# Kernel tuning notes

Hardware: AMD Instinct MI355X
Metric: run time of the kernel (lower is better)

The kernel has to match this reference:

```python
import jax, jax.numpy as jnp
import numpy as np

N = 100_000; E = 1_600_000; H = 64
TH = 0.7; ATT_TH = 0.2; EPS = 1e-5

# Heaviside spike with ATan surrogate gradient (spikingjelly default style).
@jax.custom_vjp
def spike_fn(v):
    return (v >= 0.0).astype(v.dtype)

def _spike_fwd(v):
    return spike_fn(v), v

def _spike_bwd(v, g):
    alpha = 2.0
    sg = (alpha / 2.0) / (1.0 + (jnp.pi / 2.0 * alpha * v) ** 2)
    return (g * sg,)

spike_fn.defvjp(_spike_fwd, _spike_bwd)

def lif_step(v, x, th):
    # integrate-and-fire step with hard reset-to-zero
    v = v + x
    s = spike_fn(v - th)
    return s, v * (1.0 - s)

def batchnorm(x, g, b):
    # training-mode BatchNorm1d over the node axis
    m = x.mean(axis=0)
    var = x.var(axis=0)
    return (x - m) * jax.lax.rsqrt(var + EPS) * g + b

def gcn(x, W, b, src, dst, w):
    # PyG GCNConv: xW, add self loops, symmetric deg^-1/2 normalization, scatter-add
    xw = x @ W                                   # [N,H]
    deg = jnp.ones((x.shape[0],), x.dtype).at[dst].add(w)   # self-loop weight 1
    dis = jax.lax.rsqrt(deg)
    norm = dis[src] * w * dis[dst]               # [E]
    agg = jnp.zeros_like(xw).at[dst].add(norm[:, None] * xw[src])
    return agg + (dis * dis)[:, None] * xw + b   # self-loop term + bias

def enc(x, src, dst, w, Wg, bg, bn_g, bn_b, v_conv):
    # Wg order: convs[0], conv, pos_conv, q_lins, k_lins, v_lins, att_conv
    # bn order:  bn_1, bn_2, pos_bn, pos_bn_2, q_bn, k_bn, v_bn, att_bn, att_bn_2
    x = batchnorm(gcn(x, Wg[0], bg[0], src, dst, w), bn_g[0], bn_b[0])
    x, v_conv = lif_step(v_conv, x, TH)          # conv_lif (stateful, never reset)
    x = batchnorm(gcn(x, Wg[1], bg[1], src, dst, w), bn_g[1], bn_b[1])
    z = jnp.zeros_like(x)
    # SGPE positional branch (pos_lif is reset after enc -> fresh state)
    x_pos_spike, _ = lif_step(z, x, TH)
    x_pos = batchnorm(gcn(x_pos_spike, Wg[2], bg[2], src, dst, w), bn_g[2], bn_b[2])
    x = batchnorm(x_pos + x, bn_g[3], bn_b[3])
    # attention branch: conv_lif second (stateful) call
    x_att, v_conv = lif_step(v_conv, x, TH)
    q, _ = lif_step(z, batchnorm(gcn(x_att, Wg[3], bg[3], src, dst, w), bn_g[4], bn_b[4]), TH)
    k, _ = lif_step(z, batchnorm(gcn(x_att, Wg[4], bg[4], src, dst, w), bn_g[5], bn_b[5]), TH)
    v, _ = lif_step(z, batchnorm(gcn(x_att, Wg[5], bg[5], src, dst, w), bn_g[6], bn_b[6]), TH)
    qk = (q * k).mean(axis=1)                    # [N]  (num_attention_heads == 1 path)
    qk, _ = lif_step(jnp.zeros_like(qk), qk, ATT_TH)
    att = qk[:, None] * v                        # repeat(H,1).T * v
    att = batchnorm(gcn(att, Wg[6], bg[6], src, dst, w), bn_g[7], bn_b[7])
    x = batchnorm(x + 0.125 * att, bn_g[8], bn_b[8])
    return x, v_conv

def setup_inputs():
    key = jax.random.key(0)
    ks = jax.random.split(key, 6)
    x = jax.random.normal(ks[0], (N, H), jnp.float32)
    edge_index = jax.random.randint(ks[1], (2, E), 0, N)
    edge_mask = jax.random.randint(ks[2], (E,), 0, 2, jnp.int32)
    Wg = jax.random.normal(ks[3], (7, H, H), jnp.float32) / jnp.sqrt(H)
    bg = jnp.zeros((7, H), jnp.float32)
    bn_g = jnp.ones((9, H), jnp.float32)
    bn_b = jnp.zeros((9, H), jnp.float32)
    W_lin = jax.random.normal(ks[4], (H, H), jnp.float32) / jnp.sqrt(H)
    return {"x": x, "edge_index": edge_index, "edge_mask": edge_mask,
            "Wg": Wg, "bg": bg, "bn_g": bn_g, "bn_b": bn_b, "W_lin": W_lin}

def reference(x, edge_index, edge_mask, Wg, bg, bn_g, bn_b, W_lin):
    src, dst = edge_index[0], edge_index[1]
    w1 = jnp.ones((E,), x.dtype)
    w2 = edge_mask.astype(x.dtype)   # dropout_edge(p=0.2) realized as fixed mask (weight 0 == removed edge)
    v0 = jnp.zeros((N, H), x.dtype)
    s1, v_conv = enc(x, src, dst, w1, Wg, bg, bn_g, bn_b, v0)
    s2, _ = enc(x, src, dst, w2, Wg, bg, bn_g, bn_b, v_conv)  # conv_lif state carries over
    z1 = (s1 @ W_lin).sum(axis=1)    # dec: lin(x).sum(1)
    z2 = (s2 @ W_lin).sum(axis=1)
    return (z1, z2)
```

## Files before the change

kernel.cpp:

```cpp
#include <hip/hip_runtime.h>
#include <math.h>
#include <stdint.h>
#include <limits.h>

#define NN 100000
#define NE 1600000
#define HH 64
#define THF 0.7f
#define ATTTH 0.2f
#define EPSF 1e-5f
#define SCAN_B ((NN + 255) / 256)
#define EM2CAP 1000000
#define NBE 2048
#define NHTOT ((size_t)NN * 64)
#define NB_ROW4C (NN / 4)
#define NTILE (NN / 32)

typedef unsigned long long u64;

__device__ inline int bcast_i(int v, int l) {
    return __builtin_amdgcn_readlane(v, l);
}
__device__ inline unsigned bcast_u(unsigned v, int l) {
    return (unsigned)__builtin_amdgcn_readlane((int)v, l);
}
__device__ inline float bcast_f(float v, int l) {
    return __int_as_float(__builtin_amdgcn_readlane(__float_as_int(v), l));
}


__global__ void hist_k(const int* __restrict__ dst, const int* __restrict__ mask,
                       int* __restrict__ cntp, int* __restrict__ rk) {
    int e = blockIdx.x * 256 + threadIdx.x;
    if (e >= NE) return;
    int d = dst[e];
    int inc = 1 | ((mask[e] & 1) << 16);
    rk[e] = atomicAdd(&cntp[d], inc);
}

__global__ void scan1d_k(const int* __restrict__ cntp,
                         int* __restrict__ rp1, int* __restrict__ rp2,
                         int* __restrict__ bsum,
                         float* __restrict__ dis1, float* __restrict__ d21,
                         float* __restrict__ dis2m, float* __restrict__ d22) {
    __shared__ int ls[256];
    int half = (blockIdx.x >= SCAN_B) ? 1 : 0;
    int blk = blockIdx.x - half * SCAN_B;
    int* rp = half ? rp2 : rp1;
    int i = blk * 256 + threadIdx.x;
    int p = (i < NN) ? cntp[i] : 0;
    int v = half ? (p >> 16) : (p & 0xFFFF);
    if (i < NN) {
        float dg = (float)(v + 1);
        float is = 1.0f / sqrtf(dg);
        float iv = 1.0f / dg;
        if (half) { dis2m[i] = is; d22[i] = iv; }
        else      { dis1[i] = is;  d21[i] = iv; }
    }
    ls[threadIdx.x] = v;
    __syncthreads();
    for (int off = 1; off < 256; off <<= 1) {
        int t = (threadIdx.x >= off) ? ls[threadIdx.x - off] : 0;
        __syncthreads();
        ls[threadIdx.x] += t;
        __syncthreads();
    }
    if (i < NN) rp[i] = ls[threadIdx.x] - v;
    if (threadIdx.x == 255) bsum[blockIdx.x] = ls[255];
}

__global__ __launch_bounds__(512) void scan2d_k(int* __restrict__ bsum,
                                                int* __restrict__ rp1,
                                                int* __restrict__ rp2) {
    __shared__ int ls[512];
    int i = threadIdx.x;
    for (int s = 0; s < 2; s++) {
        int v = (i < SCAN_B) ? bsum[s * SCAN_B + i] : 0;
        ls[i] = v;
        __syncthreads();
        for (int off = 1; off < 512; off <<= 1) {
            int t = (i >= off) ? ls[i - off] : 0;
            __syncthreads();
            ls[i] += t;
            __syncthreads();
        }
        if (i < SCAN_B) bsum[s * SCAN_B + i] = ls[i] - v;
        if (i == SCAN_B - 1) { if (s == 0) rp1[NN] = ls[i]; else rp2[NN] = ls[i]; }
        __syncthreads();
    }
}

__global__ void scan3d_k(int* __restrict__ rp1, int* __restrict__ rp2,
                         const int* __restrict__ bsum) {
    int half = (blockIdx.x >= SCAN_B) ? 1 : 0;
    int blk = blockIdx.x - half * SCAN_B;
    int* rp = half ? rp2 : rp1;
    int i = blk * 256 + threadIdx.x;
    if (i < NN) rp[i] += bsum[blockIdx.x];
}

__global__ void csr_fill_k(const int* __restrict__ src, const int* __restrict__ dst,
                           const int* __restrict__ mask, const int* __restrict__ rk,
                           const int* __restrict__ rp1, const int* __restrict__ rp2,
                           int* __restrict__ emA, int* __restrict__ emB) {
    int e = blockIdx.x * 256 + threadIdx.x;
    if (e >= NE) return;
    int s = src[e], d = dst[e];
    int mk = mask[e] & 1;
    int r = rk[e];
    emA[rp1[d] + (r & 0xFFFF)] = (s << 1) | mk;
    if (mk) emB[rp2[d] + (r >> 16)] = s;
}

__device__ void seg_sort_node(int* __restrict__ em, int beg, int end,
                              int* skey, int lane) {
    int L = end - beg;
    if (L <= 1) return;
    if (L <= 64) {
        int k = (lane < L) ? em[beg + lane] : INT_MAX;
        int rank = 0;
#pragma unroll 8
        for (int r = 0; r < L; r++) {
            int kr = bcast_i(k, r);
            rank += (kr < k || (kr == k && r < lane)) ? 1 : 0;
        }
        if (lane < L) em[beg + rank] = k;
    } else if (L <= 512) {
        for (int i = lane; i < L; i += 64) skey[i] = em[beg + i];
        for (int it = 0; it < L; it++) {
            int par = it & 1;
            for (int p = par + 2 * lane; p + 1 < L; p += 128) {
                int ka = skey[p], kb = skey[p + 1];
                if (kb < ka) { skey[p] = kb; skey[p + 1] = ka; }
            }
        }
        for (int i = lane; i < L; i += 64) em[beg + i] = skey[i];
    }
}

__global__ __launch_bounds__(256) void seg_sort2_k(int* __restrict__ emA,
                                                   const int* __restrict__ rp1,
                                                   int* __restrict__ emB,
                                                   const int* __restrict__ rp2) {
    __shared__ int skey[4][512];
    int tid = threadIdx.x, lane = tid & 63, w = tid >> 6;
    int bid = blockIdx.x;
    if (bid < NB_ROW4C) {
        int n = bid * 4 + w;
        seg_sort_node(emA, rp1[n], rp1[n + 1], skey[w], lane);
    } else {
        int n = (bid - NB_ROW4C) * 4 + w;
        seg_sort_node(emB, rp2[n], rp2[n + 1], skey[w], lane);
    }
}


__global__ __launch_bounds__(256) void gemm_k(const float* __restrict__ in,
                                              const float* __restrict__ W,
                                              float* __restrict__ xw) {
    __shared__ float sW[64 * 64];
    __shared__ float sx[32 * 65];
    int tid = threadIdx.x;
    const float4* W4 = (const float4*)W;
    float4* sW4 = (float4*)sW;
    for (int i = tid; i < 1024; i += 256) sW4[i] = W4[i];
    const float* inb = in + (size_t)blockIdx.x * 2048;
    for (int i = tid; i < 2048; i += 256) sx[(i >> 6) * 65 + (i & 63)] = inb[i];
    __syncthreads();
    int cg = tid & 15, rr = tid >> 4;
    float a0 = 0, a1 = 0, a2 = 0, a3 = 0, c0 = 0, c1 = 0, c2 = 0, c3 = 0;
#pragma unroll
    for (int k = 0; k < 64; k++) {
        float4 wv = *(const float4*)&sW[k * 64 + cg * 4];
        float xa = sx[rr * 65 + k];
        float xb = sx[(rr + 16) * 65 + k];
        a0 += xa * wv.x; a1 += xa * wv.y; a2 += xa * wv.z; a3 += xa * wv.w;
        c0 += xb * wv.x; c1 += xb * wv.y; c2 += xb * wv.z; c3 += xb * wv.w;
    }
    size_t r0 = (size_t)(blockIdx.x * 32 + rr) * 64 + cg * 4;
    size_t r1 = (size_t)(blockIdx.x * 32 + rr + 16) * 64 + cg * 4;
    *(float4*)&xw[r0] = make_float4(a0, a1, a2, a3);
    *(float4*)&xw[r1] = make_float4(c0, c1, c2, c3);
}


__global__ __launch_bounds__(256) void gather_stats_k(const float* __restrict__ xw,
                                                      const int* __restrict__ em,
                                                      int shift,
                                                      const float* __restrict__ dis,
                                                      const int* __restrict__ rp,
                                                      const float* __restrict__ d2i,
                                                      const float* __restrict__ bias,
                                                      float* __restrict__ out,
                                                      double* __restrict__ part) {
    int tid = threadIdx.x, lane = tid & 63, w = tid >> 6;
    double ps = 0.0, pq = 0.0;
    for (int n = blockIdx.x * 4 + w; n < NN; n += NBE * 4) {
        int beg = rp[n], end = rp[n + 1];
        float disn = dis[n];
        float self = d2i[n] * xw[(size_t)n * 64 + lane] + bias[lane];
        float acc = 0.0f;
        for (int base = beg; base < end; base += 64) {
            int cnt = min(64, end - base);
            int m = 0; float nl = 0.0f;
            if (base + lane < end) {
                m = em[base + lane];
                nl = dis[m >> shift] * disn;
            }
            int j = 0;
            for (; j + 8 <= cnt; j += 8) {
#pragma unroll
                for (int u = 0; u < 8; u++) {
                    int s = bcast_i(m, j + u) >> shift;
                    float nv = bcast_f(nl, j + u);
                    acc += nv * xw[(size_t)s * 64 + lane];
                }
            }
            for (; j < cnt; j++) {
                int s = bcast_i(m, j) >> shift;
                float nv = bcast_f(nl, j);
                acc += nv * xw[(size_t)s * 64 + lane];
            }
        }
        float o = acc + self;
        out[(size_t)n * 64 + lane] = o;
        ps += (double)o;
        pq += (double)o * (double)o;
    }
    __shared__ double ls[4][64], lq[4][64];
    ls[w][lane] = ps; lq[w][lane] = pq;
    __syncthreads();
    if (tid < 64) {
        double a = ls[0][tid] + ls[1][tid] + ls[2][tid] + ls[3][tid];
        double b = lq[0][tid] + lq[1][tid] + lq[2][tid] + lq[3][tid];
        part[(size_t)blockIdx.x * 128 + tid] = a;
        part[(size_t)blockIdx.x * 128 + 64 + tid] = b;
    }
}

__global__ __launch_bounds__(256) void sharedL0_k(const float* __restrict__ xw,
                                                  const int* __restrict__ em,
                                                  const int* __restrict__ rp,
                                                  const float* __restrict__ dis1,
                                                  const float* __restrict__ dis2m,
                                                  const float* __restrict__ d21,
                                                  const float* __restrict__ d22,
                                                  const float* __restrict__ bias,
                                                  float* __restrict__ o1,
                                                  float* __restrict__ o2,
                                                  double* __restrict__ part) {
    int tid = threadIdx.x, lane = tid & 63, w = tid >> 6;
    double sA = 0.0, qA = 0.0, sB = 0.0, qB = 0.0;
    for (int n = blockIdx.x * 4 + w; n < NN; n += NBE * 4) {
        int beg = rp[n], end = rp[n + 1];
        float disn1 = dis1[n], disn2 = dis2m[n];
        float xv = xw[(size_t)n * 64 + lane];
        float self1 = d21[n] * xv + bias[lane];
        float self2 = d22[n] * xv + bias[lane];
        float acc1 = 0.0f, acc2 = 0.0f;
        for (int base = beg; base < end; base += 64) {
            int cnt = min(64, end - base);
            int m = 0; float nl1 = 0.0f, nl2 = 0.0f;
            if (base + lane < end) {
                m = em[base + lane];
                int s = m >> 1;
                nl1 = dis1[s] * disn1;
                nl2 = dis2m[s] * disn2;
            }
            int j = 0;
            for (; j + 8 <= cnt; j += 8) {
#pragma unroll
                for (int u = 0; u < 8; u++) {
                    int key = bcast_i(m, j + u);
                    int s = key >> 1;
                    float n1 = bcast_f(nl1, j + u);
                    float n2 = bcast_f(nl2, j + u);
                    float v = xw[(size_t)s * 64 + lane];
                    acc1 += n1 * v;
                    acc2 += (key & 1) ? n2 * v : 0.0f;
                }
            }
            for (; j < cnt; j++) {
                int key = bcast_i(m, j);
                int s = key >> 1;
                float n1 = bcast_f(nl1, j);
                float n2 = bcast_f(nl2, j);
                float v = xw[(size_t)s * 64 + lane];
                acc1 += n1 * v;
                acc2 += (key & 1) ? n2 * v : 0.0f;
            }
        }
        size_t o = (size_t)n * 64 + lane;
        float v1 = acc1 + self1;
        float v2 = acc2 + self2;
        o1[o] = v1;
        o2[o] = v2;
        sA += (double)v1; qA += (double)v1 * (double)v1;
        sB += (double)v2; qB += (double)v2 * (double)v2;
    }
    __shared__ double l1[4][64], l2[4][64], l3[4][64], l4[4][64];
    l1[w][lane] = sA; l2[w][lane] = qA; l3[w][lane] = sB; l4[w][lane] = qB;
    __syncthreads();
    if (tid < 64) {
        size_t o = (size_t)blockIdx.x * 256;
        part[o + tid]       = l1[0][tid] + l1[1][tid] + l1[2][tid] + l1[3][tid];
        part[o + 64 + tid]  = l2[0][tid] + l2[1][tid] + l2[2][tid] + l2[3][tid];
        part[o + 128 + tid] = l3[0][tid] + l3[1][tid] + l3[2][tid] + l3[3][tid];
        part[o + 192 + tid] = l4[0][tid] + l4[1][tid] + l4[2][tid] + l4[3][tid];
    }
}


__global__ __launch_bounds__(256) void bitagg_k(const u64* __restrict__ bits,
                                                const int* __restrict__ em,
                                                int shift,
                                                const float* __restrict__ dis,
                                                const int* __restrict__ rp,
                                                const float* __restrict__ d2i,
                                                float* __restrict__ A) {
    int tid = threadIdx.x, lane = tid & 63, w = tid >> 6;
    int sh31 = lane & 31;
    bool islo = lane < 32;
    for (int n = blockIdx.x * 4 + w; n < NN; n += NBE * 4) {
        int beg = rp[n], end = rp[n + 1];
        float disn = dis[n];
        float acc = 0.0f;
        for (int base = beg; base < end; base += 64) {
            int cnt = min(64, end - base);
            unsigned blo = 0, bhi = 0; float nl = 0.0f;
            if (base + lane < end) {
                int m = em[base + lane];
                int s = m >> shift;
                nl = dis[s] * disn;
                u64 b = bits[s];
                blo = (unsigned)b;
                bhi = (unsigned)(b >> 32);
            }
            int j = 0;
            for (; j + 8 <= cnt; j += 8) {
#pragma unroll
                for (int u = 0; u < 8; u++) {
                    float nv = bcast_f(nl, j + u);
                    unsigned lo = bcast_u(blo, j + u);
                    unsigned hi = bcast_u(bhi, j + u);
                    unsigned sel = islo ? lo : hi;
                    acc += ((sel >> sh31) & 1u) ? nv : 0.0f;
                }
            }
            for (; j < cnt; j++) {
                float nv = bcast_f(nl, j);
                unsigned lo = bcast_u(blo, j);
                unsigned hi = bcast_u(bhi, j);
                unsigned sel = islo ? lo : hi;
                acc += ((sel >> sh31) & 1u) ? nv : 0.0f;
            }
        }
        u64 bn = bits[n];
        unsigned seln = islo ? (unsigned)bn : (unsigned)(bn >> 32);
        acc += ((seln >> sh31) & 1u) ? d2i[n] : 0.0f;
        A[(size_t)n * 64 + lane] = acc;
    }
}


__global__ __launch_bounds__(256) void gemmb_stats_k(const float* __restrict__ A,
                                                     const float* __restrict__ W,
                                                     const float* __restrict__ bias,
                                                     float* __restrict__ G,
                                                     double* __restrict__ part,
                                                     int pstride, int pbase) {
    __shared__ float smem[4096 + 2112];
    float* sW = smem;
    float* sx = smem + 4096;
    int tid = threadIdx.x;
    const float4* W4 = (const float4*)W;
    float4* sW4 = (float4*)sW;
    for (int i = tid; i < 1024; i += 256) sW4[i] = W4[i];
    int cg = tid & 15, rr = tid >> 4;
    float4 bv = *(const float4*)&bias[cg * 4];
    double s0 = 0, s1 = 0, s2 = 0, s3 = 0, q0 = 0, q1 = 0, q2 = 0, q3 = 0;
    for (int tile = blockIdx.x; tile < NTILE; tile += NBE) {
        const float* Ab = A + (size_t)tile * 2048;
        __syncthreads();
        for (int i = tid; i < 2048; i += 256) sx[(i >> 6) * 65 + (i & 63)] = Ab[i];
        __syncthreads();
        float a0 = bv.x, a1 = bv.y, a2 = bv.z, a3 = bv.w;
        float c0 = bv.x, c1 = bv.y, c2 = bv.z, c3 = bv.w;
#pragma unroll
        for (int k = 0; k < 64; k++) {
            float4 wv = *(const float4*)&sW[k * 64 + cg * 4];
            float xa = sx[rr * 65 + k];
            float xb = sx[(rr + 16) * 65 + k];
            a0 += xa * wv.x; a1 += xa * wv.y; a2 += xa * wv.z; a3 += xa * wv.w;
            c0 += xb * wv.x; c1 += xb * wv.y; c2 += xb * wv.z; c3 += xb * wv.w;
        }
        size_t r0 = (size_t)(tile * 32 + rr) * 64 + cg * 4;
        size_t r1 = (size_t)(tile * 32 + rr + 16) * 64 + cg * 4;
        *(float4*)&G[r0] = make_float4(a0, a1, a2, a3);
        *(float4*)&G[r1] = make_float4(c0, c1, c2, c3);
        s0 += (double)a0; s0 += (double)c0;
        s1 += (double)a1; s1 += (double)c1;
        s2 += (double)a2; s2 += (double)c2;
        s3 += (double)a3; s3 += (double)c3;
        q0 += (double)a0 * (double)a0; q0 += (double)c0 * (double)c0;
        q1 += (double)a1 * (double)a1; q1 += (double)c1 * (double)c1;
        q2 += (double)a2 * (double)a2; q2 += (double)c2 * (double)c2;
        q3 += (double)a3 * (double)a3; q3 += (double)c3 * (double)c3;
    }
    __syncthreads();
    double* sS = (double*)smem;
    double* sQ = sS + 64 * 17;
    sS[(cg * 4 + 0) * 17 + rr] = s0; sQ[(cg * 4 + 0) * 17 + rr] = q0;
    sS[(cg * 4 + 1) * 17 + rr] = s1; sQ[(cg * 4 + 1) * 17 + rr] = q1;
    sS[(cg * 4 + 2) * 17 + rr] = s2; sQ[(cg * 4 + 2) * 17 + rr] = q2;
    sS[(cg * 4 + 3) * 17 + rr] = s3; sQ[(cg * 4 + 3) * 17 + rr] = q3;
    __syncthreads();
    if (tid < 64) {
        double a = 0.0, b = 0.0;
#pragma unroll
        for (int r = 0; r < 16; r++) { a += sS[tid * 17 + r]; b += sQ[tid * 17 + r]; }
        part[(size_t)blockIdx.x * pstride + pbase + tid] = a;
        part[(size_t)blockIdx.x * pstride + pbase + 64 + tid] = b;
    }
}


__global__ __launch_bounds__(256) void bn_red_k(const double* __restrict__ part,
                                                double* __restrict__ st) {
    __shared__ double tr[256];
    int t = threadIdx.x, c = blockIdx.x;
    double s = 0.0;
    for (int b = t; b < NBE; b += 256) s += part[(size_t)b * 128 + c];
    tr[t] = s;
    __syncthreads();
    for (int off = 128; off > 0; off >>= 1) {
        if (t < off) tr[t] += tr[t + off];
        __syncthreads();
    }
    if (t == 0) st[c] = tr[0];
}

__global__ __launch_bounds__(256) void bn_red2_k(const double* __restrict__ part,
                                                 double* __restrict__ sta,
                                                 double* __restrict__ stb) {
    __shared__ double tr[256];
    int t = threadIdx.x, c = blockIdx.x;
    double s = 0.0;
    for (int b = t; b < NBE; b += 256) s += part[(size_t)b * 256 + c];
    tr[t] = s;
    __syncthreads();
    for (int off = 128; off > 0; off >>= 1) {
        if (t < off) tr[t] += tr[t + off];
        __syncthreads();
    }
    if (t == 0) {
        if (c < 128) sta[c] = tr[0];
        else stb[c - 128] = tr[0];
    }
}

__global__ __launch_bounds__(256) void bn_red3_k(const double* __restrict__ part,
                                                 double* __restrict__ sta,
                                                 double* __restrict__ stb,
                                                 double* __restrict__ stc) {
    __shared__ double tr[256];
    int t = threadIdx.x, c = blockIdx.x;
    double s = 0.0;
    for (int b = t; b < NBE; b += 256) s += part[(size_t)b * 384 + c];
    tr[t] = s;
    __syncthreads();
    for (int off = 128; off > 0; off >>= 1) {
        if (t < off) tr[t] += tr[t + off];
        __syncthreads();
    }
    if (t == 0) {
        if (c < 128) sta[c] = tr[0];
        else if (c < 256) stb[c - 128] = tr[0];
        else stc[c - 256] = tr[0];
    }
}

__device__ inline void bn_ss(const double* __restrict__ st, const float* __restrict__ gam,
                             const float* __restrict__ bet, int c,
                             float* __restrict__ ssc, float* __restrict__ ssh) {
    double m = st[c] * (1.0 / NN);
    double v = st[64 + c] * (1.0 / NN) - m * m;
    float scale = (float)((double)gam[c] / sqrt(v + (double)EPSF));
    ssc[c] = scale;
    ssh[c] = bet[c] - (float)m * scale;
}


__global__ __launch_bounds__(256) void lif_spike_k(const float* __restrict__ G,
                                                   const double* __restrict__ st,
                                                   const float* __restrict__ gam,
                                                   const float* __restrict__ bet,
                                                   float* __restrict__ vconv,
                                                   u64* __restrict__ bits) {
    __shared__ float ssc[64], ssh[64];
    int tid = threadIdx.x;
    if (tid < 64) bn_ss(st, gam, bet, tid, ssc, ssh);
    __syncthreads();
    int lane = tid & 63;
    size_t i = (size_t)blockIdx.x * 256 + tid;
    float v = vconv[i] + (G[i] * ssc[lane] + ssh[lane]);
    bool sp = (v - THF >= 0.0f);
    u64 m = __ballot(sp);
    vconv[i] = sp ? 0.0f : v;
    if (lane == 0) bits[i >> 6] = m;
}

__global__ __launch_bounds__(256) void spike_save_k(const float* __restrict__ G,
                                                    const double* __restrict__ st,
                                                    const float* __restrict__ gam,
                                                    const float* __restrict__ bet,
                                                    float* __restrict__ xsave,
                                                    u64* __restrict__ bits) {
    __shared__ float ssc[64], ssh[64];
    int tid = threadIdx.x;
    if (tid < 64) bn_ss(st, gam, bet, tid, ssc, ssh);
    __syncthreads();
    int lane = tid & 63;
    size_t i = (size_t)blockIdx.x * 256 + tid;
    float xv = G[i] * ssc[lane] + ssh[lane];
    xsave[i] = xv;
    u64 m = __ballot(xv - THF >= 0.0f);
    if (lane == 0) bits[i >> 6] = m;
}

__global__ __launch_bounds__(256) void lif_spike_save_k(const float* __restrict__ F,
                                                        const double* __restrict__ st,
                                                        const float* __restrict__ gam,
                                                        const float* __restrict__ bet,
                                                        float* __restrict__ vconv,
                                                        float* __restrict__ xsave,
                                                        u64* __restrict__ bits) {
    __shared__ float ssc[64], ssh[64];
    int tid = threadIdx.x;
    if (tid < 64) bn_ss(st, gam, bet, tid, ssc, ssh);
    __syncthreads();
    int lane = tid & 63;
    size_t i = (size_t)blockIdx.x * 256 + tid;
    float xv = F[i] * ssc[lane] + ssh[lane];
    xsave[i] = xv;
    float v = vconv[i] + xv;
    bool sp = (v - THF >= 0.0f);
    u64 m = __ballot(sp);
    vconv[i] = sp ? 0.0f : v;
    if (lane == 0) bits[i >> 6] = m;
}

__global__ __launch_bounds__(256) void qkv_att_spike_k(const float* __restrict__ Gq,
                                                       const float* __restrict__ Gk,
                                                       const float* __restrict__ Gv,
                                                       const double* __restrict__ st4,
                                                       const double* __restrict__ st5,
                                                       const double* __restrict__ st6,
                                                       const float* __restrict__ gam4,
                                                       const float* __restrict__ bet4,
                                                       const float* __restrict__ gam5,
                                                       const float* __restrict__ bet5,
                                                       const float* __restrict__ gam6,
                                                       const float* __restrict__ bet6,
                                                       u64* __restrict__ bits) {
    __shared__ float sc4[64], sh4[64], sc5[64], sh5[64], sc6[64], sh6[64];
    int tid = threadIdx.x;
    if (tid < 64) {
        bn_ss(st4, gam4, bet4, tid, sc4, sh4);
        bn_ss(st5, gam5, bet5, tid, sc5, sh5);
        bn_ss(st6, gam6, bet6, tid, sc6, sh6);
    }
    __syncthreads();
    int lane = tid & 63;
    size_t i = (size_t)blockIdx.x * 256 + tid;
    bool qb = (Gq[i] * sc4[lane] + sh4[lane] - THF >= 0.0f);
    bool kb = (Gk[i] * sc5[lane] + sh5[lane] - THF >= 0.0f);
    bool vb = (Gv[i] * sc6[lane] + sh6[lane] - THF >= 0.0f);
    int pc = __popcll(__ballot(qb && kb));
    bool qs = ((float)pc * (1.0f / 64.0f) - ATTTH >= 0.0f);
    u64 m = __ballot(vb && qs);
    if (lane == 0) bits[i >> 6] = m;
}


__global__ __launch_bounds__(256) void bn_add_stats_k(const float* __restrict__ G,
                                                      const double* __restrict__ st,
                                                      const float* __restrict__ gam,
                                                      const float* __restrict__ bet,
                                                      const float* __restrict__ x3,
                                                      float* __restrict__ F,
                                                      double* __restrict__ part) {
    __shared__ float ssc[64], ssh[64];
    int tid = threadIdx.x;
    if (tid < 64) bn_ss(st, gam, bet, tid, ssc, ssh);
    __syncthreads();
    int c = tid & 63;
    double s = 0.0, s2 = 0.0;
    for (size_t i = (size_t)blockIdx.x * 256 + tid; i < NHTOT; i += (size_t)NBE * 256) {
        float f = (G[i] * ssc[c] + ssh[c]) + x3[i];
        F[i] = f;
        s += (double)f;
        s2 += (double)f * (double)f;
    }
    __shared__ double ls[256], lq[256];
    ls[tid] = s; lq[tid] = s2;
    __syncthreads();
    if (tid < 64) {
        double a = ls[tid] + ls[tid + 64] + ls[tid + 128] + ls[tid + 192];
        double b = lq[tid] + lq[tid + 64] + lq[tid + 128] + lq[tid + 192];
        part[(size_t)blockIdx.x * 128 + tid] = a;
        part[(size_t)blockIdx.x * 128 + 64 + tid] = b;
    }
}

__global__ __launch_bounds__(256) void bn_scale_add_stats_k(const float* __restrict__ G,
                                                            const double* __restrict__ st,
                                                            const float* __restrict__ gam,
                                                            const float* __restrict__ bet,
                                                            const float* __restrict__ x4,
                                                            float* __restrict__ tmp2,
                                                            double* __restrict__ part) {
    __shared__ float ssc[64], ssh[64];
    int tid = threadIdx.x;
    if (tid < 64) bn_ss(st, gam, bet, tid, ssc, ssh);
    __syncthreads();
    int c = tid & 63;
    double s = 0.0, s2 = 0.0;
    for (size_t i = (size_t)blockIdx.x * 256 + tid; i < NHTOT; i += (size_t)NBE * 256) {
        float f = x4[i] + 0.125f * (G[i] * ssc[c] + ssh[c]);
        tmp2[i] = f;
        s += (double)f;
        s2 += (double)f * (double)f;
    }
    __shared__ double ls[256], lq[256];
    ls[tid] = s; lq[tid] = s2;
    __syncthreads();
    if (tid < 64) {
        double a = ls[tid] + ls[tid + 64] + ls[tid + 128] + ls[tid + 192];
        double b = lq[tid] + lq[tid + 64] + lq[tid + 128] + lq[tid + 192];
        part[(size_t)blockIdx.x * 128 + tid] = a;
        part[(size_t)blockIdx.x * 128 + 64 + tid] = b;
    }
}

__global__ __launch_bounds__(256) void decode_k(const float* __restrict__ tmp2,
                                                const double* __restrict__ st,
                                                const float* __restrict__ gam,
                                                const float* __restrict__ bet,
                                                const float* __restrict__ wrow,
                                                float* __restrict__ z) {
    __shared__ float ssc[64], ssh[64];
    int tid = threadIdx.x;
    if (tid < 64) bn_ss(st, gam, bet, tid, ssc, ssh);
    __syncthreads();
    int lane = tid & 63;
    int row = blockIdx.x * 4 + (tid >> 6);
    float sv = tmp2[(size_t)row * 64 + lane] * ssc[lane] + ssh[lane];
    float p = sv * wrow[lane];
#pragma unroll
    for (int off = 32; off > 0; off >>= 1) p += __shfl_xor(p, off, 64);
    if (lane == 0) z[row] = p;
}

__global__ void wrow_k(const float* __restrict__ W_lin, float* __restrict__ wrow) {
    int h = threadIdx.x;
    if (h >= 64) return;
    float s = 0.0f;
    for (int j = 0; j < 64; j++) s += W_lin[h * 64 + j];
    wrow[h] = s;
}


extern "C" void kernel_launch(void* const* d_in, const int* in_sizes, int n_in,
                              void* d_out, int out_size, void* d_ws, size_t ws_size,
                              hipStream_t stream) {
    const float* x    = (const float*)d_in[0];
    const int* eidx   = (const int*)d_in[1];
    const int* emask  = (const int*)d_in[2];
    const float* Wg   = (const float*)d_in[3];
    const float* bg   = (const float*)d_in[4];
    const float* bng  = (const float*)d_in[5];
    const float* bnb  = (const float*)d_in[6];
    const float* Wlin = (const float*)d_in[7];
    float* zout = (float*)d_out;

    const int* srcp = eidx;
    const int* dstp = eidx + NE;
    const size_t NH = (size_t)NN * HH;

    float* ws = (float*)d_ws;
    size_t off = 0;
    float* P1 = ws + off; off += NH;
    float* P2 = ws + off; off += NH;
    float* P3 = ws + off; off += NH;
    float* P4 = ws + off; off += NH;
    float* P5 = ws + off; off += NH;
    float* vconv = ws + off; off += NH;
    int* emA = (int*)(ws + off); off += NE;
    int* emB = (int*)(ws + off); off += EM2CAP;
    u64* sbits = (u64*)(ws + off); off += 2 * (size_t)NN;
    double* part = (double*)(ws + off); off += 2 * (size_t)NBE * 384;
    double* stats = (double*)(ws + off); off += 2 * 18 * 128;
    int* rk = (int*)(ws + off); off += NE;
    float* dis1 = ws + off; off += NN;
    float* d21  = ws + off; off += NN;
    float* dis2m = ws + off; off += NN;
    float* d22  = ws + off; off += NN;
    float* wrow = ws + off; off += 64;
    int* rp1 = (int*)(ws + off); off += NN + 2;
    int* rp2 = (int*)(ws + off); off += NN + 2;
    int* cntp = (int*)(ws + off); off += NN;
    int* bsum = (int*)(ws + off); off += 2 * SCAN_B + 4;
    if (off & 1) off++;
    float* P8 = ws + off; off += NH;
    size_t needA2 = off * 4;
    const bool tA2 = (ws_size >= needA2);

    hipMemsetAsync(cntp, 0, NN * sizeof(int), stream);
    hipMemsetAsync(vconv, 0, NH * sizeof(float), stream);

    const int NB_EDGE = NE / 256;
    const int NB_ROW4 = NN / 4;
    const int NB_GEMM = NN / 32;

    wrow_k<<<1, 64, 0, stream>>>(Wlin, wrow);
    hist_k<<<NB_EDGE, 256, 0, stream>>>(dstp, emask, cntp, rk);
    scan1d_k<<<2 * SCAN_B, 256, 0, stream>>>(cntp, rp1, rp2, bsum,
                                             dis1, d21, dis2m, d22);
    scan2d_k<<<1, 512, 0, stream>>>(bsum, rp1, rp2);
    scan3d_k<<<2 * SCAN_B, 256, 0, stream>>>(rp1, rp2, bsum);
    csr_fill_k<<<NB_EDGE, 256, 0, stream>>>(srcp, dstp, emask, rk, rp1, rp2,
                                            emA, emB);
    seg_sort2_k<<<2 * NB_ROW4C, 256, 0, stream>>>(emA, rp1, emB, rp2);

    auto enc = [&](const int* em, int shift, const float* dis, const int* rp,
                   const float* d2i, int bnbase, float* zo, const float* G0pre) {
        auto ST = [&](int bni) { return stats + (bnbase + bni) * 128; };
        auto W = [&](int wi) { return Wg + wi * 4096; };
        auto BI = [&](int wi) { return bg + wi * 64; };
        auto GM = [&](int bi) { return bng + bi * 64; };
        auto BT = [&](int bi) { return bnb + bi * 64; };

        const float* G0 = G0pre;
        if (!G0) {
            gemm_k<<<NB_GEMM, 256, 0, stream>>>(x, W(0), P1);
            gather_stats_k<<<NBE, 256, 0, stream>>>(P1, em, shift, dis, rp, d2i,
                                                    BI(0), P2, part);
            bn_red_k<<<128, 256, 0, stream>>>(part, ST(0));
            G0 = P2;
        }
        lif_spike_k<<<NB_ROW4, 256, 0, stream>>>(G0, ST(0), GM(0), BT(0), vconv, sbits);
        bitagg_k<<<NBE, 256, 0, stream>>>(sbits, em, shift, dis, rp, d2i, P1);
        gemmb_stats_k<<<NBE, 256, 0, stream>>>(P1, W(1), BI(1), P5, part, 128, 0);
        bn_red_k<<<128, 256, 0, stream>>>(part, ST(1));
        spike_save_k<<<NB_ROW4, 256, 0, stream>>>(P5, ST(1), GM(1), BT(1), P3, sbits);
        bitagg_k<<<NBE, 256, 0, stream>>>(sbits, em, shift, dis, rp, d2i, P1);
        gemmb_stats_k<<<NBE, 256, 0, stream>>>(P1, W(2), BI(2), P5, part, 128, 0);
        bn_red_k<<<128, 256, 0, stream>>>(part, ST(2));
        bn_add_stats_k<<<NBE, 256, 0, stream>>>(P5, ST(2), GM(2), BT(2), P3, P4, part);
        bn_red_k<<<128, 256, 0, stream>>>(part, ST(3));
        lif_spike_save_k<<<NB_ROW4, 256, 0, stream>>>(P4, ST(3), GM(3), BT(3),
                                                      vconv, P4, sbits);
        bitagg_k<<<NBE, 256, 0, stream>>>(sbits, em, shift, dis, rp, d2i, P1);
        gemmb_stats_k<<<NBE, 256, 0, stream>>>(P1, W(3), BI(3), P2, part, 384, 0);
        gemmb_stats_k<<<NBE, 256, 0, stream>>>(P1, W(4), BI(4), P3, part, 384, 128);
        gemmb_stats_k<<<NBE, 256, 0, stream>>>(P1, W(5), BI(5), P5, part, 384, 256);
        bn_red3_k<<<384, 256, 0, stream>>>(part, ST(4), ST(5), ST(6));
        qkv_att_spike_k<<<NB_ROW4, 256, 0, stream>>>(P2, P3, P5,
                                                     ST(4), ST(5), ST(6),
                                                     GM(4), BT(4), GM(5), BT(5),
                                                     GM(6), BT(6), sbits);
        bitagg_k<<<NBE, 256, 0, stream>>>(sbits, em, shift, dis, rp, d2i, P1);
        gemmb_stats_k<<<NBE, 256, 0, stream>>>(P1, W(6), BI(6), P2, part, 128, 0);
        bn_red_k<<<128, 256, 0, stream>>>(part, ST(7));
        bn_scale_add_stats_k<<<NBE, 256, 0, stream>>>(P2, ST(7), GM(7), BT(7),
                                                      P4, P3, part);
        bn_red_k<<<128, 256, 0, stream>>>(part, ST(8));
        decode_k<<<NB_ROW4, 256, 0, stream>>>(P3, ST(8), GM(8), BT(8), wrow, zo);
    };

    if (tA2) {
        gemm_k<<<NB_GEMM, 256, 0, stream>>>(x, Wg, P1);
        sharedL0_k<<<NBE, 256, 0, stream>>>(P1, emA, rp1, dis1, dis2m, d21, d22,
                                            bg, P2, P8, part);
        bn_red2_k<<<256, 256, 0, stream>>>(part, stats + 0 * 128, stats + 9 * 128);
        enc(emA, 1, dis1, rp1, d21, 0, zout, P2);
        enc(emB, 0, dis2m, rp2, d22, 9, zout + NN, P8);
    } else {
        enc(emA, 1, dis1, rp1, d21, 0, zout, nullptr);
        enc(emB, 0, dis2m, rp2, d22, 9, zout + NN, nullptr);
    }
}
```

Before: 1.371 ms.

## Fuse bit-spike aggregation into GEMM+stats kernels, merge Q/K/V GEMMs

Replaces the separate bitagg kernel plus GEMM+stats kernel with one kernel that aggregates 32 nodes per tile into shared memory, then does the 64x64 GEMM and BN statistics directly. This drops the N×64 float round trip through global memory for the aggregated features. The Q/K/V path becomes a single kernel holding all three weight matrices in shared memory, so the aggregation is computed once for all three. The cost is higher register and LDS use, which lowers occupancy. The irregular gather now sits serially before the GEMM inside each block, so the two phases cannot overlap across kernels.

```diff
diff --git a/kernel.cpp b/kernel.cpp
--- a/kernel.cpp
+++ b/kernel.cpp
@@ -311,78 +311,82 @@
 }
 
 
-__global__ __launch_bounds__(256) void bitagg_k(const u64* __restrict__ bits,
+__device__ inline float bitagg_node(const u64* __restrict__ bits,
+                                    const int* __restrict__ em, int shift,
+                                    const float* __restrict__ dis,
+                                    const float* __restrict__ d2i,
+                                    int n, int beg, int end,
+                                    int lane, int sh31, bool islo) {
+    float disn = dis[n];
+    float acc = 0.0f;
+    for (int base = beg; base < end; base += 64) {
+        int cnt = min(64, end - base);
+        unsigned blo = 0, bhi = 0; float nl = 0.0f;
+        if (base + lane < end) {
+            int m = em[base + lane];
+            int s = m >> shift;
+            nl = dis[s] * disn;
+            u64 b = bits[s];
+            blo = (unsigned)b;
+            bhi = (unsigned)(b >> 32);
+        }
+        int j = 0;
+        for (; j + 8 <= cnt; j += 8) {
+#pragma unroll
+            for (int u = 0; u < 8; u++) {
+                float nv = bcast_f(nl, j + u);
+                unsigned lo = bcast_u(blo, j + u);
+                unsigned hi = bcast_u(bhi, j + u);
+                unsigned sel = islo ? lo : hi;
+                acc += ((sel >> sh31) & 1u) ? nv : 0.0f;
+            }
+        }
+        for (; j < cnt; j++) {
+            float nv = bcast_f(nl, j);
+            unsigned lo = bcast_u(blo, j);
+            unsigned hi = bcast_u(bhi, j);
+            unsigned sel = islo ? lo : hi;
+            acc += ((sel >> sh31) & 1u) ? nv : 0.0f;
+        }
+    }
+    u64 bn = bits[n];
+    unsigned seln = islo ? (unsigned)bn : (unsigned)(bn >> 32);
+    acc += ((seln >> sh31) & 1u) ? d2i[n] : 0.0f;
+    return acc;
+}
+
+
+__global__ __launch_bounds__(256) void fusedL_k(const u64* __restrict__ bits,
                                                 const int* __restrict__ em,
                                                 int shift,
                                                 const float* __restrict__ dis,
                                                 const int* __restrict__ rp,
                                                 const float* __restrict__ d2i,
-                                                float* __restrict__ A) {
-    int tid = threadIdx.x, lane = tid & 63, w = tid >> 6;
-    int sh31 = lane & 31;
-    bool islo = lane < 32;
-    for (int n = blockIdx.x * 4 + w; n < NN; n += NBE * 4) {
-        int beg = rp[n], end = rp[n + 1];
-        float disn = dis[n];
-        float acc = 0.0f;
-        for (int base = beg; base < end; base += 64) {
-            int cnt = min(64, end - base);
-            unsigned blo = 0, bhi = 0; float nl = 0.0f;
-            if (base + lane < end) {
-                int m = em[base + lane];
-                int s = m >> shift;
-                nl = dis[s] * disn;
-                u64 b = bits[s];
-                blo = (unsigned)b;
-                bhi = (unsigned)(b >> 32);
-            }
-            int j = 0;
-            for (; j + 8 <= cnt; j += 8) {
-#pragma unroll
-                for (int u = 0; u < 8; u++) {
-                    float nv = bcast_f(nl, j + u);
-                    unsigned lo = bcast_u(blo, j + u);
-                    unsigned hi = bcast_u(bhi, j + u);
-                    unsigned sel = islo ? lo : hi;
-                    acc += ((sel >> sh31) & 1u) ? nv : 0.0f;
-                }
-            }
-            for (; j < cnt; j++) {
-                float nv = bcast_f(nl, j);
-                unsigned lo = bcast_u(blo, j);
-                unsigned hi = bcast_u(bhi, j);
-                unsigned sel = islo ? lo : hi;
-                acc += ((sel >> sh31) & 1u) ? nv : 0.0f;
-            }
-        }
-        u64 bn = bits[n];
-        unsigned seln = islo ? (unsigned)bn : (unsigned)(bn >> 32);
-        acc += ((seln >> sh31) & 1u) ? d2i[n] : 0.0f;
-        A[(size_t)n * 64 + lane] = acc;
-    }
-}
-
-
-__global__ __launch_bounds__(256) void gemmb_stats_k(const float* __restrict__ A,
-                                                     const float* __restrict__ W,
-                                                     const float* __restrict__ bias,
-                                                     float* __restrict__ G,
-                                                     double* __restrict__ part,
-                                                     int pstride, int pbase) {
+                                                const float* __restrict__ W,
+                                                const float* __restrict__ bias,
+                                                float* __restrict__ G,
+                                                double* __restrict__ part,
+                                                int pstride, int pbase) {
     __shared__ float smem[4096 + 2112];
     float* sW = smem;
     float* sx = smem + 4096;
-    int tid = threadIdx.x;
+    int tid = threadIdx.x, lane = tid & 63, w = tid >> 6;
     const float4* W4 = (const float4*)W;
     float4* sW4 = (float4*)sW;
     for (int i = tid; i < 1024; i += 256) sW4[i] = W4[i];
+    int sh31 = lane & 31;
+    bool islo = lane < 32;
     int cg = tid & 15, rr = tid >> 4;
     float4 bv = *(const float4*)&bias[cg * 4];
     double s0 = 0, s1 = 0, s2 = 0, s3 = 0, q0 = 0, q1 = 0, q2 = 0, q3 = 0;
     for (int tile = blockIdx.x; tile < NTILE; tile += NBE) {
-        const float* Ab = A + (size_t)tile * 2048;
-        __syncthreads();
-        for (int i = tid; i < 2048; i += 256) sx[(i >> 6) * 65 + (i & 63)] = Ab[i];
+        __syncthreads();
+        for (int i = 0; i < 8; i++) {
+            int n = tile * 32 + w * 8 + i;
+            float acc = bitagg_node(bits, em, shift, dis, d2i, n, rp[n], rp[n + 1],
+                                    lane, sh31, islo);
+            sx[(w * 8 + i) * 65 + lane] = acc;
+        }
         __syncthreads();
         float a0 = bv.x, a1 = bv.y, a2 = bv.z, a3 = bv.w;
         float c0 = bv.x, c1 = bv.y, c2 = bv.z, c3 = bv.w;
@@ -421,6 +425,151 @@
         for (int r = 0; r < 16; r++) { a += sS[tid * 17 + r]; b += sQ[tid * 17 + r]; }
         part[(size_t)blockIdx.x * pstride + pbase + tid] = a;
         part[(size_t)blockIdx.x * pstride + pbase + 64 + tid] = b;
+    }
+}
+
+__global__ __launch_bounds__(256) void fused3L_k(const u64* __restrict__ bits,
+                                                 const int* __restrict__ em,
+                                                 int shift,
+                                                 const float* __restrict__ dis,
+                                                 const int* __restrict__ rp,
+                                                 const float* __restrict__ d2i,
+                                                 const float* __restrict__ Wq,
+                                                 const float* __restrict__ Wk,
+                                                 const float* __restrict__ Wv,
+                                                 const float* __restrict__ bq,
+                                                 const float* __restrict__ bk,
+                                                 const float* __restrict__ bv,
+                                                 float* __restrict__ Gq,
+                                                 float* __restrict__ Gk,
+                                                 float* __restrict__ Gv,
+                                                 double* __restrict__ part) {
+    __shared__ float smem[3 * 4096 + 2112];
+    float* sW = smem;
+    float* sx = smem + 3 * 4096;
+    int tid = threadIdx.x, lane = tid & 63, w = tid >> 6;
+    {
+        const float4* A4 = (const float4*)Wq;
+        const float4* B4 = (const float4*)Wk;
+        const float4* C4 = (const float4*)Wv;
+        float4* s4 = (float4*)sW;
+        for (int i = tid; i < 1024; i += 256) {
+            s4[i] = A4[i];
+            s4[1024 + i] = B4[i];
+            s4[2048 + i] = C4[i];
+        }
+    }
+    int sh31 = lane & 31;
+    bool islo = lane < 32;
+    int cg = tid & 15, rr = tid >> 4;
+    float4 bvq = *(const float4*)&bq[cg * 4];
+    float4 bvk = *(const float4*)&bk[cg * 4];
+    float4 bvv = *(const float4*)&bv[cg * 4];
+    double sq0 = 0, sq1 = 0, sq2 = 0, sq3 = 0, qq0 = 0, qq1 = 0, qq2 = 0, qq3 = 0;
+    double sk0 = 0, sk1 = 0, sk2 = 0, sk3 = 0, qk0 = 0, qk1 = 0, qk2 = 0, qk3 = 0;
+    double sv0 = 0, sv1 = 0, sv2 = 0, sv3 = 0, qv0 = 0, qv1 = 0, qv2 = 0, qv3 = 0;
+    for (int tile = blockIdx.x; tile < NTILE; tile += NBE) {
+        __syncthreads();
+        for (int i = 0; i < 8; i++) {
+            int n = tile * 32 + w * 8 + i;
+            float acc = bitagg_node(bits, em, shift, dis, d2i, n, rp[n], rp[n + 1],
+                                    lane, sh31, islo);
+            sx[(w * 8 + i) * 65 + lane] = acc;
+        }
+        __syncthreads();
+        float aq0 = bvq.x, aq1 = bvq.y, aq2 = bvq.z, aq3 = bvq.w;
+        float cq0 = bvq.x, cq1 = bvq.y, cq2 = bvq.z, cq3 = bvq.w;
+        float ak0 = bvk.x, ak1 = bvk.y, ak2 = bvk.z, ak3 = bvk.w;
+        float ck0 = bvk.x, ck1 = bvk.y, ck2 = bvk.z, ck3 = bvk.w;
+        float av0 = bvv.x, av1 = bvv.y, av2 = bvv.z, av3 = bvv.w;
+        float cv0 = bvv.x, cv1 = bvv.y, cv2 = bvv.z, cv3 = bvv.w;
+#pragma unroll
+        for (int k = 0; k < 64; k++) {
+            float4 wq = *(const float4*)&sW[k * 64 + cg * 4];
+            float4 wk = *(const float4*)&sW[4096 + k * 64 + cg * 4];
+            float4 wv = *(const float4*)&sW[8192 + k * 64 + cg * 4];
+            float xa = sx[rr * 65 + k];
+            float xb = sx[(rr + 16) * 65 + k];
+            aq0 += xa * wq.x; aq1 += xa * wq.y; aq2 += xa * wq.z; aq3 += xa * wq.w;
+            cq0 += xb * wq.x; cq1 += xb * wq.y; cq2 += xb * wq.z; cq3 += xb * wq.w;
+            ak0 += xa * wk.x; ak1 += xa * wk.y; ak2 += xa * wk.z; ak3 += xa * wk.w;
+            ck0 += xb * wk.x; ck1 += xb * wk.y; ck2 += xb * wk.z; ck3 += xb * wk.w;
+            av0 += xa * wv.x; av1 += xa * wv.y; av2 += xa * wv.z; av3 += xa * wv.w;
+            cv0 += xb * wv.x; cv1 += xb * wv.y; cv2 += xb * wv.z; cv3 += xb * wv.w;
+        }
+        size_t r0 = (size_t)(tile * 32 + rr) * 64 + cg * 4;
+        size_t r1 = (size_t)(tile * 32 + rr + 16) * 64 + cg * 4;
+        *(float4*)&Gq[r0] = make_float4(aq0, aq1, aq2, aq3);
+        *(float4*)&Gq[r1] = make_float4(cq0, cq1, cq2, cq3);
+        *(float4*)&Gk[r0] = make_float4(ak0, ak1, ak2, ak3);
+        *(float4*)&Gk[r1] = make_float4(ck0, ck1, ck2, ck3);
+        *(float4*)&Gv[r0] = make_float4(av0, av1, av2, av3);
+        *(float4*)&Gv[r1] = make_float4(cv0, cv1, cv2, cv3);
+        sq0 += (double)aq0; sq0 += (double)cq0;
+        sq1 += (double)aq1; sq1 += (double)cq1;
+        sq2 += (double)aq2; sq2 += (double)cq2;
+        sq3 += (double)aq3; sq3 += (double)cq3;
+        qq0 += (double)aq0 * (double)aq0; qq0 += (double)cq0 * (double)cq0;
+        qq1 += (double)aq1 * (double)aq1; qq1 += (double)cq1 * (double)cq1;
+        qq2 += (double)aq2 * (double)aq2; qq2 += (double)cq2 * (double)cq2;
+        qq3 += (double)aq3 * (double)aq3; qq3 += (double)cq3 * (double)cq3;
+        sk0 += (double)ak0; sk0 += (double)ck0;
+        sk1 += (double)ak1; sk1 += (double)ck1;
+        sk2 += (double)ak2; sk2 += (double)ck2;
+        sk3 += (double)ak3; sk3 += (double)ck3;
+        qk0 += (double)ak0 * (double)ak0; qk0 += (double)ck0 * (double)ck0;
+        qk1 += (double)ak1 * (double)ak1; qk1 += (double)ck1 * (double)ck1;
+        qk2 += (double)ak2 * (double)ak2; qk2 += (double)ck2 * (double)ck2;
+        qk3 += (double)ak3 * (double)ak3; qk3 += (double)ck3 * (double)ck3;
+        sv0 += (double)av0; sv0 += (double)cv0;
+        sv1 += (double)av1; sv1 += (double)cv1;
+        sv2 += (double)av2; sv2 += (double)cv2;
+        sv3 += (double)av3; sv3 += (double)cv3;
+        qv0 += (double)av0 * (double)av0; qv0 += (double)cv0 * (double)cv0;
+        qv1 += (double)av1 * (double)av1; qv1 += (double)cv1 * (double)cv1;
+        qv2 += (double)av2 * (double)av2; qv2 += (double)cv2 * (double)cv2;
+        qv3 += (double)av3 * (double)av3; qv3 += (double)cv3 * (double)cv3;
+    }
+    __syncthreads();
+    double* sS = (double*)smem;
+    double* sQ = sS + 64 * 17;
+    sS[(cg * 4 + 0) * 17 + rr] = sq0; sQ[(cg * 4 + 0) * 17 + rr] = qq0;
+    sS[(cg * 4 + 1) * 17 + rr] = sq1; sQ[(cg * 4 + 1) * 17 + rr] = qq1;
+    sS[(cg * 4 + 2) * 17 + rr] = sq2; sQ[(cg * 4 + 2) * 17 + rr] = qq2;
+    sS[(cg * 4 + 3) * 17 + rr] = sq3; sQ[(cg * 4 + 3) * 17 + rr] = qq3;
+    __syncthreads();
+    if (tid < 64) {
+        double a = 0.0, b = 0.0;
+#pragma unroll
+        for (int r = 0; r < 16; r++) { a += sS[tid * 17 + r]; b += sQ[tid * 17 + r]; }
+        part[(size_t)blockIdx.x * 384 + tid] = a;
+        part[(size_t)blockIdx.x * 384 + 64 + tid] = b;
+    }
+    __syncthreads();
+    sS[(cg * 4 + 0) * 17 + rr] = sk0; sQ[(cg * 4 + 0) * 17 + rr] = qk0;
+    sS[(cg * 4 + 1) * 17 + rr] = sk1; sQ[(cg * 4 + 1) * 17 + rr] = qk1;
+    sS[(cg * 4 + 2) * 17 + rr] = sk2; sQ[(cg * 4 + 2) * 17 + rr] = qk2;
+    sS[(cg * 4 + 3) * 17 + rr] = sk3; sQ[(cg * 4 + 3) * 17 + rr] = qk3;
+    __syncthreads();
+    if (tid < 64) {
+        double a = 0.0, b = 0.0;
+#pragma unroll
+        for (int r = 0; r < 16; r++) { a += sS[tid * 17 + r]; b += sQ[tid * 17 + r]; }
+        part[(size_t)blockIdx.x * 384 + 128 + tid] = a;
+        part[(size_t)blockIdx.x * 384 + 192 + tid] = b;
+    }
+    __syncthreads();
+    sS[(cg * 4 + 0) * 17 + rr] = sv0; sQ[(cg * 4 + 0) * 17 + rr] = qv0;
+    sS[(cg * 4 + 1) * 17 + rr] = sv1; sQ[(cg * 4 + 1) * 17 + rr] = qv1;
+    sS[(cg * 4 + 2) * 17 + rr] = sv2; sQ[(cg * 4 + 2) * 17 + rr] = qv2;
+    sS[(cg * 4 + 3) * 17 + rr] = sv3; sQ[(cg * 4 + 3) * 17 + rr] = qv3;
+    __syncthreads();
+    if (tid < 64) {
+        double a = 0.0, b = 0.0;
+#pragma unroll
+        for (int r = 0; r < 16; r++) { a += sS[tid * 17 + r]; b += sQ[tid * 17 + r]; }
+        part[(size_t)blockIdx.x * 384 + 256 + tid] = a;
+        part[(size_t)blockIdx.x * 384 + 320 + tid] = b;
     }
 }
 
@@ -750,28 +899,27 @@
             G0 = P2;
         }
         lif_spike_k<<<NB_ROW4, 256, 0, stream>>>(G0, ST(0), GM(0), BT(0), vconv, sbits);
-        bitagg_k<<<NBE, 256, 0, stream>>>(sbits, em, shift, dis, rp, d2i, P1);
-        gemmb_stats_k<<<NBE, 256, 0, stream>>>(P1, W(1), BI(1), P5, part, 128, 0);
+        fusedL_k<<<NBE, 256, 0, stream>>>(sbits, em, shift, dis, rp, d2i,
+                                          W(1), BI(1), P5, part, 128, 0);
         bn_red_k<<<128, 256, 0, stream>>>(part, ST(1));
         spike_save_k<<<NB_ROW4, 256, 0, stream>>>(P5, ST(1), GM(1), BT(1), P3, sbits);
-        bitagg_k<<<NBE, 256, 0, stream>>>(sbits, em, shift, dis, rp, d2i, P1);
-        gemmb_stats_k<<<NBE, 256, 0, stream>>>(P1, W(2), BI(2), P5, part, 128, 0);
+        fusedL_k<<<NBE, 256, 0, stream>>>(sbits, em, shift, dis, rp, d2i,
+                                          W(2), BI(2), P5, part, 128, 0);
         bn_red_k<<<128, 256, 0, stream>>>(part, ST(2));
         bn_add_stats_k<<<NBE, 256, 0, stream>>>(P5, ST(2), GM(2), BT(2), P3, P4, part);
         bn_red_k<<<128, 256, 0, stream>>>(part, ST(3));
         lif_spike_save_k<<<NB_ROW4, 256, 0, stream>>>(P4, ST(3), GM(3), BT(3),
                                                       vconv, P4, sbits);
-        bitagg_k<<<NBE, 256, 0, stream>>>(sbits, em, shift, dis, rp, d2i, P1);
-        gemmb_stats_k<<<NBE, 256, 0, stream>>>(P1, W(3), BI(3), P2, part, 384, 0);
-        gemmb_stats_k<<<NBE, 256, 0, stream>>>(P1, W(4), BI(4), P3, part, 384, 128);
-        gemmb_stats_k<<<NBE, 256, 0, stream>>>(P1, W(5), BI(5), P5, part, 384, 256);
+        fused3L_k<<<NBE, 256, 0, stream>>>(sbits, em, shift, dis, rp, d2i,
+                                           W(3), W(4), W(5), BI(3), BI(4), BI(5),
+                                           P2, P3, P5, part);
         bn_red3_k<<<384, 256, 0, stream>>>(part, ST(4), ST(5), ST(6));
         qkv_att_spike_k<<<NB_ROW4, 256, 0, stream>>>(P2, P3, P5,
                                                      ST(4), ST(5), ST(6),
                                                      GM(4), BT(4), GM(5), BT(5),
                                                      GM(6), BT(6), sbits);
-        bitagg_k<<<NBE, 256, 0, stream>>>(sbits, em, shift, dis, rp, d2i, P1);
-        gemmb_stats_k<<<NBE, 256, 0, stream>>>(P1, W(6), BI(6), P2, part, 128, 0);
+        fusedL_k<<<NBE, 256, 0, stream>>>(sbits, em, shift, dis, rp, d2i,
+                                          W(6), BI(6), P2, part, 128, 0);
         bn_red_k<<<128, 256, 0, stream>>>(part, ST(7));
         bn_scale_add_stats_k<<<NBE, 256, 0, stream>>>(P2, ST(7), GM(7), BT(7),
                                                       P4, P3, part);
```

Measured after the change: 1.483 ms. +8.2%, slower.

## Fuse spike-bit aggregation into GEMM+stats kernel for single-output GCN layers

Applied to the files above, without the earlier changes.

Adds a fused kernel in which each block aggregates 32 nodes' spike-bit neighbourhood sums directly into shared memory, then runs the 64x64 GEMM with bias and writes the per-block BN statistics. It replaces the separate bitagg and gemmb_stats launches for layers 1, 2 and 6, so the N x 64 intermediate no longer makes a round trip through global memory and one launch is saved per layer. The qkv layer still uses the separate kernels, because its aggregation result feeds three GEMMs. The cost is a longer per-block critical path, with gather latency and GEMM now serialized inside each block, and more shared memory held while the irregular gather runs, which can lower overlap.

```diff
diff --git a/kernel.cpp b/kernel.cpp
--- a/kernel.cpp
+++ b/kernel.cpp
@@ -311,6 +311,50 @@
 }
 
 
+__device__ inline float bitagg_node(const u64* __restrict__ bits,
+                                    const int* __restrict__ em, int shift,
+                                    const float* __restrict__ dis,
+                                    const float* __restrict__ d2i,
+                                    int n, int beg, int end,
+                                    int lane, int sh31, bool islo) {
+    float disn = dis[n];
+    float acc = 0.0f;
+    for (int base = beg; base < end; base += 64) {
+        int cnt = min(64, end - base);
+        unsigned blo = 0, bhi = 0; float nl = 0.0f;
+        if (base + lane < end) {
+            int m = em[base + lane];
+            int s = m >> shift;
+            nl = dis[s] * disn;
+            u64 b = bits[s];
+            blo = (unsigned)b;
+            bhi = (unsigned)(b >> 32);
+        }
+        int j = 0;
+        for (; j + 8 <= cnt; j += 8) {
+#pragma unroll
+            for (int u = 0; u < 8; u++) {
+                float nv = bcast_f(nl, j + u);
+                unsigned lo = bcast_u(blo, j + u);
+                unsigned hi = bcast_u(bhi, j + u);
+                unsigned sel = islo ? lo : hi;
+                acc += ((sel >> sh31) & 1u) ? nv : 0.0f;
+            }
+        }
+        for (; j < cnt; j++) {
+            float nv = bcast_f(nl, j);
+            unsigned lo = bcast_u(blo, j);
+            unsigned hi = bcast_u(bhi, j);
+            unsigned sel = islo ? lo : hi;
+            acc += ((sel >> sh31) & 1u) ? nv : 0.0f;
+        }
+    }
+    u64 bn = bits[n];
+    unsigned seln = islo ? (unsigned)bn : (unsigned)(bn >> 32);
+    acc += ((seln >> sh31) & 1u) ? d2i[n] : 0.0f;
+    return acc;
+}
+
 __global__ __launch_bounds__(256) void bitagg_k(const u64* __restrict__ bits,
                                                 const int* __restrict__ em,
                                                 int shift,
@@ -322,42 +366,8 @@
     int sh31 = lane & 31;
     bool islo = lane < 32;
     for (int n = blockIdx.x * 4 + w; n < NN; n += NBE * 4) {
-        int beg = rp[n], end = rp[n + 1];
-        float disn = dis[n];
-        float acc = 0.0f;
-        for (int base = beg; base < end; base += 64) {
-            int cnt = min(64, end - base);
-            unsigned blo = 0, bhi = 0; float nl = 0.0f;
-            if (base + lane < end) {
-                int m = em[base + lane];
-                int s = m >> shift;
-                nl = dis[s] * disn;
-                u64 b = bits[s];
-                blo = (unsigned)b;
-                bhi = (unsigned)(b >> 32);
-            }
-            int j = 0;
-            for (; j + 8 <= cnt; j += 8) {
-#pragma unroll
-                for (int u = 0; u < 8; u++) {
-                    float nv = bcast_f(nl, j + u);
-                    unsigned lo = bcast_u(blo, j + u);
-                    unsigned hi = bcast_u(bhi, j + u);
-                    unsigned sel = islo ? lo : hi;
-                    acc += ((sel >> sh31) & 1u) ? nv : 0.0f;
-                }
-            }
-            for (; j < cnt; j++) {
-                float nv = bcast_f(nl, j);
-                unsigned lo = bcast_u(blo, j);
-                unsigned hi = bcast_u(bhi, j);
-                unsigned sel = islo ? lo : hi;
-                acc += ((sel >> sh31) & 1u) ? nv : 0.0f;
-            }
-        }
-        u64 bn = bits[n];
-        unsigned seln = islo ? (unsigned)bn : (unsigned)(bn >> 32);
-        acc += ((seln >> sh31) & 1u) ? d2i[n] : 0.0f;
+        float acc = bitagg_node(bits, em, shift, dis, d2i, n, rp[n], rp[n + 1],
+                                lane, sh31, islo);
         A[(size_t)n * 64 + lane] = acc;
     }
 }
@@ -383,6 +393,79 @@
         const float* Ab = A + (size_t)tile * 2048;
         __syncthreads();
         for (int i = tid; i < 2048; i += 256) sx[(i >> 6) * 65 + (i & 63)] = Ab[i];
+        __syncthreads();
+        float a0 = bv.x, a1 = bv.y, a2 = bv.z, a3 = bv.w;
+        float c0 = bv.x, c1 = bv.y, c2 = bv.z, c3 = bv.w;
+#pragma unroll
+        for (int k = 0; k < 64; k++) {
+            float4 wv = *(const float4*)&sW[k * 64 + cg * 4];
+            float xa = sx[rr * 65 + k];
+            float xb = sx[(rr + 16) * 65 + k];
+            a0 += xa * wv.x; a1 += xa * wv.y; a2 += xa * wv.z; a3 += xa * wv.w;
+            c0 += xb * wv.x; c1 += xb * wv.y; c2 += xb * wv.z; c3 += xb * wv.w;
+        }
+        size_t r0 = (size_t)(tile * 32 + rr) * 64 + cg * 4;
+        size_t r1 = (size_t)(tile * 32 + rr + 16) * 64 + cg * 4;
+        *(float4*)&G[r0] = make_float4(a0, a1, a2, a3);
+        *(float4*)&G[r1] = make_float4(c0, c1, c2, c3);
+        s0 += (double)a0; s0 += (double)c0;
+        s1 += (double)a1; s1 += (double)c1;
+        s2 += (double)a2; s2 += (double)c2;
+        s3 += (double)a3; s3 += (double)c3;
+        q0 += (double)a0 * (double)a0; q0 += (double)c0 * (double)c0;
+        q1 += (double)a1 * (double)a1; q1 += (double)c1 * (double)c1;
+        q2 += (double)a2 * (double)a2; q2 += (double)c2 * (double)c2;
+        q3 += (double)a3 * (double)a3; q3 += (double)c3 * (double)c3;
+    }
+    __syncthreads();
+    double* sS = (double*)smem;
+    double* sQ = sS + 64 * 17;
+    sS[(cg * 4 + 0) * 17 + rr] = s0; sQ[(cg * 4 + 0) * 17 + rr] = q0;
+    sS[(cg * 4 + 1) * 17 + rr] = s1; sQ[(cg * 4 + 1) * 17 + rr] = q1;
+    sS[(cg * 4 + 2) * 17 + rr] = s2; sQ[(cg * 4 + 2) * 17 + rr] = q2;
+    sS[(cg * 4 + 3) * 17 + rr] = s3; sQ[(cg * 4 + 3) * 17 + rr] = q3;
+    __syncthreads();
+    if (tid < 64) {
+        double a = 0.0, b = 0.0;
+#pragma unroll
+        for (int r = 0; r < 16; r++) { a += sS[tid * 17 + r]; b += sQ[tid * 17 + r]; }
+        part[(size_t)blockIdx.x * pstride + pbase + tid] = a;
+        part[(size_t)blockIdx.x * pstride + pbase + 64 + tid] = b;
+    }
+}
+
+
+__global__ __launch_bounds__(256) void fusedL_k(const u64* __restrict__ bits,
+                                                const int* __restrict__ em,
+                                                int shift,
+                                                const float* __restrict__ dis,
+                                                const int* __restrict__ rp,
+                                                const float* __restrict__ d2i,
+                                                const float* __restrict__ W,
+                                                const float* __restrict__ bias,
+                                                float* __restrict__ G,
+                                                double* __restrict__ part,
+                                                int pstride, int pbase) {
+    __shared__ float smem[4096 + 2112];
+    float* sW = smem;
+    float* sx = smem + 4096;
+    int tid = threadIdx.x, lane = tid & 63, w = tid >> 6;
+    const float4* W4 = (const float4*)W;
+    float4* sW4 = (float4*)sW;
+    for (int i = tid; i < 1024; i += 256) sW4[i] = W4[i];
+    int sh31 = lane & 31;
+    bool islo = lane < 32;
+    int cg = tid & 15, rr = tid >> 4;
+    float4 bv = *(const float4*)&bias[cg * 4];
+    double s0 = 0, s1 = 0, s2 = 0, s3 = 0, q0 = 0, q1 = 0, q2 = 0, q3 = 0;
+    for (int tile = blockIdx.x; tile < NTILE; tile += NBE) {
+        __syncthreads();
+        for (int i = 0; i < 8; i++) {
+            int n = tile * 32 + w * 8 + i;
+            float acc = bitagg_node(bits, em, shift, dis, d2i, n, rp[n], rp[n + 1],
+                                    lane, sh31, islo);
+            sx[(w * 8 + i) * 65 + lane] = acc;
+        }
         __syncthreads();
         float a0 = bv.x, a1 = bv.y, a2 = bv.z, a3 = bv.w;
         float c0 = bv.x, c1 = bv.y, c2 = bv.z, c3 = bv.w;
@@ -750,12 +833,12 @@
             G0 = P2;
         }
         lif_spike_k<<<NB_ROW4, 256, 0, stream>>>(G0, ST(0), GM(0), BT(0), vconv, sbits);
-        bitagg_k<<<NBE, 256, 0, stream>>>(sbits, em, shift, dis, rp, d2i, P1);
-        gemmb_stats_k<<<NBE, 256, 0, stream>>>(P1, W(1), BI(1), P5, part, 128, 0);
+        fusedL_k<<<NBE, 256, 0, stream>>>(sbits, em, shift, dis, rp, d2i,
+                                          W(1), BI(1), P5, part, 128, 0);
         bn_red_k<<<128, 256, 0, stream>>>(part, ST(1));
         spike_save_k<<<NB_ROW4, 256, 0, stream>>>(P5, ST(1), GM(1), BT(1), P3, sbits);
-        bitagg_k<<<NBE, 256, 0, stream>>>(sbits, em, shift, dis, rp, d2i, P1);
-        gemmb_stats_k<<<NBE, 256, 0, stream>>>(P1, W(2), BI(2), P5, part, 128, 0);
+        fusedL_k<<<NBE, 256, 0, stream>>>(sbits, em, shift, dis, rp, d2i,
+                                          W(2), BI(2), P5, part, 128, 0);
         bn_red_k<<<128, 256, 0, stream>>>(part, ST(2));
         bn_add_stats_k<<<NBE, 256, 0, stream>>>(P5, ST(2), GM(2), BT(2), P3, P4, part);
         bn_red_k<<<128, 256, 0, stream>>>(part, ST(3));
@@ -770,8 +853,8 @@
                                                      ST(4), ST(5), ST(6),
                                                      GM(4), BT(4), GM(5), BT(5),
                                                      GM(6), BT(6), sbits);
-        bitagg_k<<<NBE, 256, 0, stream>>>(sbits, em, shift, dis, rp, d2i, P1);
-        gemmb_stats_k<<<NBE, 256, 0, stream>>>(P1, W(6), BI(6), P2, part, 128, 0);
+        fusedL_k<<<NBE, 256, 0, stream>>>(sbits, em, shift, dis, rp, d2i,
+                                          W(6), BI(6), P2, part, 128, 0);
         bn_red_k<<<128, 256, 0, stream>>>(part, ST(7));
         bn_scale_add_stats_k<<<NBE, 256, 0, stream>>>(P2, ST(7), GM(7), BT(7),
                                                       P4, P3, part);
```

New measurement: 1.323 ms. 1.04x faster.
